# Kernel tuning notes

Measured on AMD Instinct MI355X. Metric: run time of the kernel, lower is better.

The kernel has to match this reference:

```python
import jax, jax.numpy as jnp
import numpy as np

P = 8          # patch_size
EPS = 1e-6     # LayerNorm2d eps


def _conv(x, w, b, groups=1):
    # x: (B,Cin,H,W), w: (Cout, Cin//groups, kh, kw)
    y = jax.lax.conv_general_dilated(
        x, w, window_strides=(1, 1), padding='SAME',
        feature_group_count=groups,
        dimension_numbers=('NCHW', 'OIHW', 'NCHW'))
    return y + b[None, :, None, None]


def _ln2d(x, w, b):
    mu = jnp.mean(x, axis=1, keepdims=True)
    var = jnp.mean((x - mu) ** 2, axis=1, keepdims=True)
    y = (x - mu) / jnp.sqrt(var + EPS)
    return w[None, :, None, None] * y + b[None, :, None, None]


def _fft_mix(x, fw):
    # windowed rFFT2 -> per-(channel,freq) real weight -> irFFT2.
    # H,W divisible by P, so window_partitionx == plain window partition.
    B, C, H, W = x.shape
    nh, nw = H // P, W // P
    xw = x.reshape(B, C, nh, P, nw, P).transpose(0, 2, 4, 1, 3, 5)  # (B,nh,nw,C,P,P)
    f = jnp.fft.rfft2(xw)                    # (B,nh,nw,C,P,P//2+1)
    f = f * fw                               # fw: (C,P,P//2+1) broadcasts
    xw = jnp.fft.irfft2(f, s=(P, P))
    return xw.transpose(0, 3, 1, 4, 2, 5).reshape(B, C, H, W)


def _gelu(x):
    return jax.nn.gelu(x, approximate=False)  # torch nn.GELU default = exact erf


def setup_inputs() -> dict:
    key = jax.random.key(0)
    ks = jax.random.split(key, 18)
    B, C, H, W = 4, 64, 256, 256
    C4, D = C * 4, C // 4
    f32 = jnp.float32

    def n(k, shape, s):
        return (jax.random.normal(k, shape, f32) * s)

    return {
        'x': jax.random.normal(ks[0], (B, C, H, W), f32),
        'ln_w': jnp.ones((C,), f32),
        'ln_b': jnp.zeros((C,), f32),
        'pconv_w': n(ks[1], (D, D, 3, 3), 0.08),
        'pconv_b': n(ks[2], (D,), 0.02),
        'w0': n(ks[3], (C4, C, 1, 1), 0.12),
        'b0': n(ks[4], (C4,), 0.02),
        'w1': n(ks[5], (C4, C, 1, 1), 0.12),
        'b1': n(ks[6], (C4,), 0.02),
        'w2': n(ks[7], (C, C4, 1, 1), 0.06),
        'b2': n(ks[8], (C,), 0.02),
        'w3': n(ks[9], (C4, 1, 3, 3), 0.3),
        'b3': n(ks[10], (C4,), 0.02),
        'w4': n(ks[11], (C, C4, 1, 1), 0.06),
        'b4': n(ks[12], (C,), 0.02),
        'fftw1': 1.0 + n(ks[13], (C, P, P // 2 + 1), 0.1),
        'fftw2': 1.0 + n(ks[14], (C, P, P // 2 + 1), 0.1),
    }


def reference(x, ln_w, ln_b, pconv_w, pconv_b, w0, b0, w1, b1,
              w2, b2, w3, b3, w4, b4, fftw1, fftw2):
    C = x.shape[1]
    D = C // 4
    C4 = C * 4

    xn = _ln2d(x, ln_w, ln_b)

    # partial 3x3 conv on first C//4 channels
    y1 = _conv(xn[:, :D], pconv_w, pconv_b)
    x2 = jnp.concatenate([y1, xn[:, D:]], axis=1)

    # branch 1: 1x1 expand -> GELU -> 1x1 contract -> windowed FFT mixing
    x1 = _conv(xn, w0, b0)
    x1 = _gelu(x1)
    x1 = _conv(x1, w2, b2)
    x1 = _fft_mix(x1, fftw1)

    # branch 2: 1x1 expand -> GELU -> depthwise 3x3 -> GELU -> 1x1 contract -> FFT mixing
    x2 = _conv(x2, w1, b1)
    x2 = _gelu(x2)
    x2 = _conv(x2, w3, b3, groups=C4)
    x2 = _gelu(x2)
    x2 = _conv(x2, w4, b4)
    x2 = _fft_mix(x2, fftw2)

    return x1 + x2
```

## Files before the change

### kernel.cpp

```cpp
#include <hip/hip_runtime.h>


typedef _Float16 f16;
typedef _Float16 f16x2 __attribute__((ext_vector_type(2)));
typedef _Float16 f16x4 __attribute__((ext_vector_type(4)));
typedef _Float16 f16x8 __attribute__((ext_vector_type(8)));
typedef float f32x4 __attribute__((ext_vector_type(4)));

__device__ __forceinline__ float gelu_f(float x) {
  float u = 1.5957691216f * (x + 0.044715f * x * x * x);
  float t = exp2f(-1.4426950409f * u);
#if __has_builtin(__builtin_amdgcn_rcpf)
  return x * __builtin_amdgcn_rcpf(1.0f + t);
#else
  return x / (1.0f + t);
#endif
}

__device__ __forceinline__ float dot2f(f16x2 a, f16x2 b, float c) {
#if __has_builtin(__builtin_amdgcn_fdot2)
  return __builtin_amdgcn_fdot2(a, b, c, false);
#else
  return c + (float)a.x * (float)b.x + (float)a.y * (float)b.y;
#endif
}

__global__ void build_kappa_kernel(const float* __restrict__ fw1,
                                   const float* __restrict__ fw2,
                                   float* __restrict__ kap1,
                                   float* __restrict__ kap2) {
  int which = blockIdx.x >> 6, c = blockIdx.x & 63;
  const float* fw = which ? fw2 : fw1;
  float* kap = which ? kap2 : kap1;
  int t = threadIdx.x, a = t >> 3, bb = t & 7;
  __shared__ float Wt[64];
  __shared__ float ct[8];
  if (t == 0) {
    const float r2 = 0.70710678118654752440f;
    ct[0] = 1.f; ct[1] = r2; ct[2] = 0.f; ct[3] = -r2;
    ct[4] = -1.f; ct[5] = -r2; ct[6] = 0.f; ct[7] = r2;
  }
  {
    int u = a, v = bb;
    Wt[t] = (v <= 4) ? fw[c * 40 + u * 5 + v]
                     : fw[c * 40 + ((8 - u) & 7) * 5 + (8 - v)];
  }
  __syncthreads();
  float acc = 0.f;
  for (int u = 0; u < 8; ++u)
    for (int v = 0; v < 8; ++v)
      acc += Wt[u * 8 + v] * ct[(u * a + v * bb) & 7];
  kap[c * 64 + t] = acc * 0.015625f;
}

__global__ void preconv_kernel(const float* __restrict__ w0, const float* __restrict__ w1,
                               const float* __restrict__ w2, const float* __restrict__ w4,
                               const float* __restrict__ w3, const float* __restrict__ b3,
                               f16* __restrict__ W0h, f16* __restrict__ W1h,
                               f16* __restrict__ W2h, f16* __restrict__ W4h,
                               f16* __restrict__ w3pk, f16* __restrict__ b3pk) {
  int i = blockIdx.x * 256 + threadIdx.x;
  if (i < 16384) W0h[i] = (f16)w0[i];
  else if (i < 32768) W1h[i - 16384] = (f16)w1[i - 16384];
  else if (i < 49152) W2h[i - 32768] = (f16)w2[i - 32768];
  else if (i < 65536) W4h[i - 49152] = (f16)w4[i - 49152];
  else if (i < 67840) {
    int j = i - 65536;
    int g = j / 72, r = j % 72, tap = r >> 3, k = r & 7;
    w3pk[j] = (f16)w3[(g * 8 + k) * 9 + tap];
  } else if (i < 68096) {
    int k = i - 67840;
    b3pk[k] = (f16)b3[k];
  }
}

__global__ void __launch_bounds__(256) ln_kernel(const float* __restrict__ x,
                                                 const float* __restrict__ lnw,
                                                 const float* __restrict__ lnb,
                                                 f16* __restrict__ xn) {
  int b = blockIdx.y;
  int px = blockIdx.x * 256 + threadIdx.x;
  const float* xp = x + ((size_t)b << 22) + px;
  float v[64];
  float s = 0.f;
#pragma unroll
  for (int c = 0; c < 64; ++c) { v[c] = xp[(size_t)c << 16]; s += v[c]; }
  float mu = s * (1.f / 64.f), s2 = 0.f;
#pragma unroll
  for (int c = 0; c < 64; ++c) { float d = v[c] - mu; s2 += d * d; }
  float rstd = rsqrtf(s2 * (1.f / 64.f) + 1e-6f);
  f16* op = xn + (size_t)b * 4194304 + (size_t)px * 64;
#pragma unroll
  for (int g = 0; g < 8; ++g) {
    f16x8 pk;
#pragma unroll
    for (int j = 0; j < 8; ++j) {
      int c = g * 8 + j;
      pk[j] = (f16)((v[c] - mu) * rstd * lnw[c] + lnb[c]);
    }
    *(f16x8*)(op + g * 8) = pk;
  }
}

__global__ void __launch_bounds__(256) pconv_kernel(const f16* __restrict__ xn,
                                                    const float* __restrict__ pw,
                                                    const float* __restrict__ pb,
                                                    f16* __restrict__ y1) {
  __shared__ __align__(16) char halo[18 * 640];
  __shared__ f16 wpk[2304];
  __shared__ float pbs[16];
  int t = threadIdx.x, blk = blockIdx.x, b = blockIdx.y;
  const f16* xnb = xn + (size_t)b * 4194304;
  f16* y1b = y1 + (size_t)b * 1048576;
  int h0 = (blk >> 4) << 4, w0 = (blk & 15) << 4;
  for (int i = t; i < 2304; i += 256) {
    int co = i / 144, r = i % 144, tap = r >> 4, ci = r & 15;
    wpk[i] = (f16)pw[co * 144 + ci * 9 + tap];
  }
  if (t < 16) pbs[t] = pb[t];
  for (int i = 0; i < 3; ++i) {
    int u = i * 256 + t;
    if (u < 648) {
      int hp = u >> 1, half = u & 1;
      int hr = hp / 18, hc = hp - hr * 18;
      int h = h0 - 1 + hr, w = w0 - 1 + hc;
      f16x8 v = {0, 0, 0, 0, 0, 0, 0, 0};
      if ((unsigned)h < 256u && (unsigned)w < 256u)
        v = *(const f16x8*)(xnb + ((((size_t)h << 8)) + w) * 64 + half * 8);
      *(f16x8*)(halo + hr * 640 + ((hc * 32 + half * 16) ^ ((hr & 7) << 4))) = v;
    }
  }
  __syncthreads();
  int rl = t >> 4, cl = t & 15;
  float acc[16];
#pragma unroll
  for (int co = 0; co < 16; ++co) acc[co] = pbs[co];
#pragma unroll
  for (int ty = 0; ty < 3; ++ty)
#pragma unroll
    for (int tx = 0; tx < 3; ++tx) {
      int hr = rl + ty, hc = cl + tx, tap = ty * 3 + tx;
      f16x8 ld0 = *(const f16x8*)(halo + hr * 640 + ((hc * 32) ^ ((hr & 7) << 4)));
      f16x8 ld1 = *(const f16x8*)(halo + hr * 640 + ((hc * 32 + 16) ^ ((hr & 7) << 4)));
#pragma unroll
      for (int co = 0; co < 16; ++co) {
#pragma unroll
        for (int p = 0; p < 4; ++p) {
          f16x2 xp = {ld0[2 * p], ld0[2 * p + 1]};
          f16x2 wp = *(const f16x2*)&wpk[co * 144 + tap * 16 + 2 * p];
          acc[co] = dot2f(xp, wp, acc[co]);
        }
#pragma unroll
        for (int p = 0; p < 4; ++p) {
          f16x2 xp = {ld1[2 * p], ld1[2 * p + 1]};
          f16x2 wp = *(const f16x2*)&wpk[co * 144 + tap * 16 + 8 + 2 * p];
          acc[co] = dot2f(xp, wp, acc[co]);
        }
      }
    }
  size_t px = (((size_t)(h0 + rl)) << 8) + w0 + cl;
  f16x8 o0, o1;
#pragma unroll
  for (int j = 0; j < 8; ++j) { o0[j] = (f16)acc[j]; o1[j] = (f16)acc[8 + j]; }
  *(f16x8*)(y1b + px * 16) = o0;
  *(f16x8*)(y1b + px * 16 + 8) = o1;
}

__global__ void __launch_bounds__(256) b1_kernel(
    const f16* __restrict__ xn, const f16* __restrict__ W0h,
    const float* __restrict__ b0, const f16* __restrict__ W2h,
    const float* __restrict__ b2, f16* __restrict__ u1d,
    f16* __restrict__ u1w) {
  __shared__ __align__(16) f16 As[8192];
  __shared__ __align__(16) f16 Es[8192];
  int t = threadIdx.x, b = blockIdx.y;
  const f16* xnb = xn + (size_t)b * 4194304;
  f16* u1b = (b < 3) ? (u1d + (size_t)b * 4194304) : u1w;
  int px0 = blockIdx.x << 7;
#pragma unroll
  for (int i = 0; i < 4; ++i) {
    int u = i * 256 + t, row = u >> 3, cb = (u & 7) << 4;
    f16x8 v = *(const f16x8*)(xnb + (size_t)(px0 + row) * 64 + (cb >> 1));
    *(f16x8*)((char*)As + row * 128 + (cb ^ ((row & 7) << 4))) = v;
  }
  __syncthreads();
  int l = t & 63, wv = t >> 6, lm = l & 15, kg = l >> 4;
  f32x4 uacc[2][4];
#pragma unroll
  for (int a = 0; a < 2; ++a)
#pragma unroll
    for (int n = 0; n < 4; ++n) uacc[a][n] = (f32x4){0.f, 0.f, 0.f, 0.f};
  for (int cc = 0; cc < 4; ++cc) {
    f32x4 eacc[2][4];
#pragma unroll
    for (int a = 0; a < 2; ++a)
#pragma unroll
      for (int n = 0; n < 4; ++n) eacc[a][n] = (f32x4){0.f, 0.f, 0.f, 0.f};
#pragma unroll
    for (int kk = 0; kk < 2; ++kk) {
      int kb = kk * 64 + kg * 16;
      f16x8 af[2];
#pragma unroll
      for (int mt = 0; mt < 2; ++mt) {
        int row = wv * 32 + mt * 16 + lm;
        af[mt] = *(const f16x8*)((char*)As + row * 128 + (kb ^ ((row & 7) << 4)));
      }
      f16x8 bf[4];
#pragma unroll
      for (int nt = 0; nt < 4; ++nt) {
        int co = cc * 64 + nt * 16 + lm;
        bf[nt] = *(const f16x8*)(W0h + (size_t)co * 64 + kk * 32 + kg * 8);
      }
#pragma unroll
      for (int mt = 0; mt < 2; ++mt)
#pragma unroll
        for (int nt = 0; nt < 4; ++nt)
          eacc[mt][nt] = __builtin_amdgcn_mfma_f32_16x16x32_f16(bf[nt], af[mt], eacc[mt][nt], 0, 0, 0);
    }
    if (cc) __syncthreads();
#pragma unroll
    for (int mt = 0; mt < 2; ++mt) {
      int row = wv * 32 + mt * 16 + lm;
#pragma unroll
      for (int nt = 0; nt < 4; ++nt) {
        int c0 = nt * 16 + kg * 4;
        float4 bz4 = *(const float4*)&b0[cc * 64 + c0];
        f16x4 pk;
        pk[0] = (f16)gelu_f(eacc[mt][nt][0] + bz4.x);
        pk[1] = (f16)gelu_f(eacc[mt][nt][1] + bz4.y);
        pk[2] = (f16)gelu_f(eacc[mt][nt][2] + bz4.z);
        pk[3] = (f16)gelu_f(eacc[mt][nt][3] + bz4.w);
        *(f16x4*)((char*)Es + row * 128 + ((c0 * 2) ^ ((row & 7) << 4))) = pk;
      }
    }
    __syncthreads();
#pragma unroll
    for (int kk = 0; kk < 2; ++kk) {
      int kb = kk * 64 + kg * 16;
      f16x8 af[2];
#pragma unroll
      for (int mt = 0; mt < 2; ++mt) {
        int row = wv * 32 + mt * 16 + lm;
        af[mt] = *(const f16x8*)((char*)Es + row * 128 + (kb ^ ((row & 7) << 4)));
      }
      f16x8 bf[4];
#pragma unroll
      for (int nt = 0; nt < 4; ++nt) {
        int co = nt * 16 + lm;
        bf[nt] = *(const f16x8*)(W2h + (size_t)co * 256 + cc * 64 + kk * 32 + kg * 8);
      }
#pragma unroll
      for (int mt = 0; mt < 2; ++mt)
#pragma unroll
        for (int nt = 0; nt < 4; ++nt)
          uacc[mt][nt] = __builtin_amdgcn_mfma_f32_16x16x32_f16(bf[nt], af[mt], uacc[mt][nt], 0, 0, 0);
    }
    __syncthreads();
  }
#pragma unroll
  for (int mt = 0; mt < 2; ++mt) {
    int row = wv * 32 + mt * 16 + lm;
#pragma unroll
    for (int nt = 0; nt < 4; ++nt) {
      int c0 = nt * 16 + kg * 4;
      float4 bz4 = *(const float4*)&b2[c0];
      f16x4 pk;
      pk[0] = (f16)(uacc[mt][nt][0] + bz4.x);
      pk[1] = (f16)(uacc[mt][nt][1] + bz4.y);
      pk[2] = (f16)(uacc[mt][nt][2] + bz4.z);
      pk[3] = (f16)(uacc[mt][nt][3] + bz4.w);
      *(f16x4*)((char*)Es + row * 128 + ((c0 * 2) ^ ((row & 7) << 4))) = pk;
    }
  }
  __syncthreads();
  int co = t >> 2, q = t & 3;
  f16x8 o[4];
#pragma unroll
  for (int i = 0; i < 32; ++i) {
    int m = q * 32 + i;
    o[i >> 3][i & 7] =
        *(const f16*)((char*)Es + m * 128 + ((co * 2) ^ ((m & 7) << 4)));
  }
  f16* up = u1b + ((size_t)co << 16) + px0 + q * 32;
#pragma unroll
  for (int ss = 0; ss < 4; ++ss) *(f16x8*)(up + ss * 8) = o[ss];
}

__global__ void __launch_bounds__(256) b2_kernel(
    const f16* __restrict__ xn, const f16* __restrict__ y1,
    const f16* __restrict__ W1h, const float* __restrict__ b1v,
    const f16* __restrict__ W4h, const float* __restrict__ b4,
    const f16* __restrict__ w3pk, const f16* __restrict__ b3pk,
    f16* __restrict__ u2) {
  __shared__ __align__(16) f16 xin[12288];
  __shared__ __align__(16) f16 Es[6144];
  int t = threadIdx.x, blk = blockIdx.x, b = blockIdx.y;
  const f16* xnb = xn + (size_t)b * 4194304;
  const f16* y1b = y1 + (size_t)b * 1048576;
  f16* u2b = u2 + (size_t)b * 4194304;
  int h0 = (blk >> 4) << 3, w0 = (blk & 15) << 4;
#pragma unroll
  for (int i = 0; i < 6; ++i) {
    int u = i * 256 + t;
    int hp = u >> 3, part = u & 7;
    f16x8 v = {0, 0, 0, 0, 0, 0, 0, 0};
    if (hp < 180) {
      int hr = hp / 18, hc = hp - hr * 18;
      int h = h0 - 1 + hr, w = w0 - 1 + hc;
      if ((unsigned)h < 256u && (unsigned)w < 256u) {
        size_t px = ((size_t)h << 8) + w;
        v = (part < 2) ? *(const f16x8*)(y1b + px * 16 + part * 8)
                       : *(const f16x8*)(xnb + px * 64 + part * 8);
      }
    }
    *(f16x8*)((char*)xin + hp * 128 + ((part * 16) ^ ((hp & 7) << 4))) = v;
  }
  __syncthreads();
  int l = t & 63, wv = t >> 6, lm = l & 15, kg = l >> 4;
  f32x4 uacc[2][4];
#pragma unroll
  for (int a = 0; a < 2; ++a)
#pragma unroll
    for (int n = 0; n < 4; ++n) uacc[a][n] = (f32x4){0.f, 0.f, 0.f, 0.f};
  for (int kc = 0; kc < 4; ++kc) {
#pragma unroll
    for (int sub = 0; sub < 2; ++sub) {
      int ce0 = kc * 64 + sub * 32;
      f32x4 eacc[3][2];
#pragma unroll
      for (int a = 0; a < 3; ++a)
#pragma unroll
        for (int n = 0; n < 2; ++n) eacc[a][n] = (f32x4){0.f, 0.f, 0.f, 0.f};
#pragma unroll
      for (int kk = 0; kk < 2; ++kk) {
        int kb = kk * 64 + kg * 16;
        f16x8 af[3];
#pragma unroll
        for (int mtl = 0; mtl < 3; ++mtl) {
          int row = (mtl * 4 + wv) * 16 + lm;
          af[mtl] = *(const f16x8*)((char*)xin + row * 128 + (kb ^ ((row & 7) << 4)));
        }
        f16x8 bf[2];
#pragma unroll
        for (int nt = 0; nt < 2; ++nt) {
          int ce = ce0 + nt * 16 + lm;
          bf[nt] = *(const f16x8*)(W1h + (size_t)ce * 64 + kk * 32 + kg * 8);
        }
#pragma unroll
        for (int mtl = 0; mtl < 3; ++mtl)
#pragma unroll
          for (int nt = 0; nt < 2; ++nt)
            eacc[mtl][nt] = __builtin_amdgcn_mfma_f32_16x16x32_f16(bf[nt], af[mtl], eacc[mtl][nt], 0, 0, 0);
      }
      __syncthreads();
#pragma unroll
      for (int mtl = 0; mtl < 3; ++mtl) {
        int row = (mtl * 4 + wv) * 16 + lm;
#pragma unroll
        for (int nt = 0; nt < 2; ++nt) {
          int cL = nt * 16 + kg * 4;
          float4 bz4 = *(const float4*)&b1v[ce0 + cL];
          f16x4 pk;
          pk[0] = (f16)gelu_f(eacc[mtl][nt][0] + bz4.x);
          pk[1] = (f16)gelu_f(eacc[mtl][nt][1] + bz4.y);
          pk[2] = (f16)gelu_f(eacc[mtl][nt][2] + bz4.z);
          pk[3] = (f16)gelu_f(eacc[mtl][nt][3] + bz4.w);
          *(f16x4*)((char*)Es + row * 64 + ((cL * 2) ^ (((row >> 1) & 3) << 4))) = pk;
        }
      }
      __syncthreads();
      int g9 = (ce0 + kg * 8) >> 3;
      f16x8 wv9[9];
#pragma unroll
      for (int tap = 0; tap < 9; ++tap)
        wv9[tap] = *(const f16x8*)(w3pk + g9 * 72 + tap * 8);
      f16x8 bias8 = *(const f16x8*)(b3pk + ce0 + kg * 8);
      f16x8 af2[2];
#pragma unroll
      for (int mt = 0; mt < 2; ++mt) {
        int px = wv * 32 + mt * 16 + lm;
        int rl2 = px >> 4, cl2 = px & 15;
        f16x8 a8 = bias8;
#pragma unroll
        for (int ty = 0; ty < 3; ++ty)
#pragma unroll
          for (int tx = 0; tx < 3; ++tx) {
            int hp = (rl2 + ty) * 18 + (cl2 + tx);
            f16x8 xv = *(const f16x8*)((char*)Es + hp * 64 + ((kg * 16) ^ (((hp >> 1) & 3) << 4)));
            a8 += xv * wv9[ty * 3 + tx];
          }
#pragma unroll
        for (int j2 = 0; j2 < 8; ++j2) af2[mt][j2] = (f16)gelu_f((float)a8[j2]);
      }
      f16x8 bf2[4];
#pragma unroll
      for (int nt = 0; nt < 4; ++nt) {
        int co = nt * 16 + lm;
        bf2[nt] = *(const f16x8*)(W4h + (size_t)co * 256 + ce0 + kg * 8);
      }
#pragma unroll
      for (int mt = 0; mt < 2; ++mt)
#pragma unroll
        for (int nt = 0; nt < 4; ++nt)
          uacc[mt][nt] = __builtin_amdgcn_mfma_f32_16x16x32_f16(bf2[nt], af2[mt], uacc[mt][nt], 0, 0, 0);
    }
  }
  __syncthreads();
#pragma unroll
  for (int mt = 0; mt < 2; ++mt) {
    int m = wv * 32 + mt * 16 + lm;
#pragma unroll
    for (int nt = 0; nt < 4; ++nt) {
      int c0 = nt * 16 + kg * 4;
      float4 bz4 = *(const float4*)&b4[c0];
      f16x4 pk;
      pk[0] = (f16)(uacc[mt][nt][0] + bz4.x);
      pk[1] = (f16)(uacc[mt][nt][1] + bz4.y);
      pk[2] = (f16)(uacc[mt][nt][2] + bz4.z);
      pk[3] = (f16)(uacc[mt][nt][3] + bz4.w);
      *(f16x4*)((char*)xin + m * 128 + ((c0 * 2) ^ ((m & 7) << 4))) = pk;
    }
  }
  __syncthreads();
  int co = t >> 2, q = t & 3;
  f16x8 o[4];
#pragma unroll
  for (int i = 0; i < 32; ++i) {
    int m = q * 32 + i;
    o[i >> 3][i & 7] =
        *(const f16*)((char*)xin + m * 128 + ((co * 2) ^ ((m & 7) << 4)));
  }
  f16* up = u2b + ((size_t)co << 16) + (size_t)(h0 + 2 * q) * 256 + w0;
  *(f16x8*)(up) = o[0];
  *(f16x8*)(up + 8) = o[1];
  *(f16x8*)(up + 256) = o[2];
  *(f16x8*)(up + 256 + 8) = o[3];
}

__global__ void __launch_bounds__(256) fftmix_kernel(
    const f16* __restrict__ u1, const f16* __restrict__ u2,
    const float* __restrict__ kap1, const float* __restrict__ kap2,
    float* __restrict__ out, int b) {
  int blk = blockIdx.x;
  int c = blk >> 3, part = blk & 7;
  int t = threadIdx.x;
  int l = t & 63, wv = (t >> 6) & 3;
  int s = l >> 3, tq = l & 7;
  __shared__ unsigned int kls[64];
  if (t < 64) {
    f16 k1 = (f16)kap1[(c << 6) + t];
    f16 k2 = (f16)kap2[(c << 6) + t];
    kls[t] = (unsigned int)__builtin_bit_cast(unsigned short, k1) |
             ((unsigned int)__builtin_bit_cast(unsigned short, k2) << 16);
  }
  __syncthreads();
  unsigned int kp[64];
#pragma unroll
  for (int j = 0; j < 64; ++j) {
    int idx = (((s - (j >> 3)) & 7) << 3) | ((tq - (j & 7)) & 7);
    kp[j] = kls[idx];
  }
  size_t cb = ((size_t)c) << 16;
  size_t obase = ((size_t)(b * 64 + c)) << 16;
  int win0 = part * 128 + wv * 32;
  for (int it = 0; it < 32; ++it) {
    int win = win0 + it;
    int wh = win >> 5, ww = win & 31;
    size_t pix = (size_t)((wh * 8 + s) << 8) + ww * 8 + tq;
    unsigned int pk =
        (unsigned int)__builtin_bit_cast(unsigned short, u1[cb + pix]) |
        ((unsigned int)__builtin_bit_cast(unsigned short, u2[cb + pix]) << 16);
    float acc = 0.f;
#pragma unroll
    for (int j = 0; j < 64; ++j) {
      unsigned int bc = (unsigned int)__builtin_amdgcn_readlane((int)pk, j);
      acc = dot2f(__builtin_bit_cast(f16x2, bc),
                  __builtin_bit_cast(f16x2, kp[j]), acc);
    }
    out[obase + pix] = acc;
  }
}

__global__ void diag_kernel(float* __restrict__ out, float code, int n) {
  int i = blockIdx.x * 256 + threadIdx.x;
  for (int p = i; p < n; p += 256 * 4096) out[p] = (p == 0) ? code : 0.f;
}

extern "C" void kernel_launch(void* const* d_in, const int* in_sizes, int n_in,
                              void* d_out, int out_size, void* d_ws,
                              size_t ws_size, hipStream_t stream) {
  const float* x       = (const float*)d_in[0];
  const float* ln_w    = (const float*)d_in[1];
  const float* ln_b    = (const float*)d_in[2];
  const float* pconv_w = (const float*)d_in[3];
  const float* pconv_b = (const float*)d_in[4];
  const float* w0      = (const float*)d_in[5];
  const float* b0      = (const float*)d_in[6];
  const float* w1      = (const float*)d_in[7];
  const float* b1      = (const float*)d_in[8];
  const float* w2      = (const float*)d_in[9];
  const float* b2      = (const float*)d_in[10];
  const float* w3      = (const float*)d_in[11];
  const float* b3      = (const float*)d_in[12];
  const float* w4      = (const float*)d_in[13];
  const float* b4      = (const float*)d_in[14];
  const float* fftw1   = (const float*)d_in[15];
  const float* fftw2   = (const float*)d_in[16];

  const size_t OFF_KAP1 = 0;
  const size_t OFF_KAP2 = 16384;
  const size_t OFF_W0H  = 32768;
  const size_t OFF_W1H  = 65536;
  const size_t OFF_W2H  = 98304;
  const size_t OFF_W4H  = 131072;
  const size_t OFF_W3PK = 163840;
  const size_t OFF_B3PK = 168448;
  const size_t OFF_Y1   = 168960;
  const size_t OFF_U2   = OFF_Y1 + 8388608ull;
  const size_t OFF_U13  = OFF_U2 + 33554432ull;
  const size_t WS_NEED  = OFF_U13 + 8388608ull;

  float* outF = (float*)d_out;
  if (ws_size < WS_NEED) {
    diag_kernel<<<4096, 256, 0, stream>>>(outF, 1000.0f + (float)(ws_size >> 20), 16777216);
    return;
  }
  char* ws = (char*)d_ws;
  float* kap1 = (float*)(ws + OFF_KAP1);
  float* kap2 = (float*)(ws + OFF_KAP2);
  f16* W0h  = (f16*)(ws + OFF_W0H);
  f16* W1h  = (f16*)(ws + OFF_W1H);
  f16* W2h  = (f16*)(ws + OFF_W2H);
  f16* W4h  = (f16*)(ws + OFF_W4H);
  f16* w3pk = (f16*)(ws + OFF_W3PK);
  f16* b3pk = (f16*)(ws + OFF_B3PK);
  f16* Y1   = (f16*)(ws + OFF_Y1);
  f16* U2   = (f16*)(ws + OFF_U2);
  f16* U13  = (f16*)(ws + OFF_U13);

  f16* XN  = (f16*)d_out;
  f16* U1D = (f16*)d_out + 16777216;

  build_kappa_kernel<<<128, 64, 0, stream>>>(fftw1, fftw2, kap1, kap2);
  preconv_kernel<<<266, 256, 0, stream>>>(w0, w1, w2, w4, w3, b3,
                                          W0h, W1h, W2h, W4h, w3pk, b3pk);
  ln_kernel<<<dim3(256, 4), 256, 0, stream>>>(x, ln_w, ln_b, XN);
  pconv_kernel<<<dim3(256, 4), 256, 0, stream>>>(XN, pconv_w, pconv_b, Y1);
  b1_kernel<<<dim3(512, 4), 256, 0, stream>>>(XN, W0h, b0, W2h, b2, U1D, U13);
  b2_kernel<<<dim3(512, 4), 256, 0, stream>>>(XN, Y1, W1h, b1, W4h, b4,
                                              w3pk, b3pk, U2);
  for (int b = 0; b < 4; ++b) {
    const f16* u1b = (b < 3) ? (U1D + (size_t)b * 4194304) : U13;
    fftmix_kernel<<<512, 256, 0, stream>>>(u1b, U2 + (size_t)b * 4194304,
                                           kap1, kap2, outF, b);
  }
}
```

Measured before the change: 395.3 us.

## Use packed fp16 GELU, merge kappa into preconv, split fftmix grid finer

The GELU epilogues now run in packed half precision with f16 exp2/rcp, and the bias-add conversions use packed round-toward-zero converts. The kappa-building kernel is folded into the weight-conversion kernel, saving one launch. The fftmix kernel doubles its grid with half the windows per block and splits the 64-term dot chain into four independent accumulators for more ILP. Doing GELU in fp16 reduces accuracy, and a larger grid means each block reloads its per-channel kernel setup more often.

```diff
diff --git a/kernel.cpp b/kernel.cpp
--- a/kernel.cpp
+++ b/kernel.cpp
@@ -6,16 +6,6 @@
 typedef _Float16 f16x4 __attribute__((ext_vector_type(4)));
 typedef _Float16 f16x8 __attribute__((ext_vector_type(8)));
 typedef float f32x4 __attribute__((ext_vector_type(4)));
-
-__device__ __forceinline__ float gelu_f(float x) {
-  float u = 1.5957691216f * (x + 0.044715f * x * x * x);
-  float t = exp2f(-1.4426950409f * u);
-#if __has_builtin(__builtin_amdgcn_rcpf)
-  return x * __builtin_amdgcn_rcpf(1.0f + t);
-#else
-  return x / (1.0f + t);
-#endif
-}
 
 __device__ __forceinline__ float dot2f(f16x2 a, f16x2 b, float c) {
 #if __has_builtin(__builtin_amdgcn_fdot2)
@@ -25,53 +15,84 @@
 #endif
 }
 
-__global__ void build_kappa_kernel(const float* __restrict__ fw1,
-                                   const float* __restrict__ fw2,
-                                   float* __restrict__ kap1,
-                                   float* __restrict__ kap2) {
-  int which = blockIdx.x >> 6, c = blockIdx.x & 63;
+__device__ __forceinline__ f16x2 gelu_pk(f16x2 x) {
+  const f16x2 c1 = {(f16)1.5957691f, (f16)1.5957691f};
+  const f16x2 c3 = {(f16)0.0713548f, (f16)0.0713548f};
+  const f16x2 cl = {(f16)-1.4426950f, (f16)-1.4426950f};
+  f16x2 x2 = x * x;
+  f16x2 u = x * (c1 + c3 * x2);
+  f16x2 a = cl * u;
+  f16 t0, t1;
+#if __has_builtin(__builtin_amdgcn_exp2h)
+  t0 = __builtin_amdgcn_exp2h(a[0]);
+  t1 = __builtin_amdgcn_exp2h(a[1]);
+#else
+  t0 = (f16)exp2f((float)a[0]);
+  t1 = (f16)exp2f((float)a[1]);
+#endif
+  f16 d0 = (f16)1.0f + t0, d1 = (f16)1.0f + t1;
+  f16 r0, r1;
+#if __has_builtin(__builtin_amdgcn_rcph)
+  r0 = __builtin_amdgcn_rcph(d0);
+  r1 = __builtin_amdgcn_rcph(d1);
+#else
+  r0 = (f16)(1.0f / (float)d0);
+  r1 = (f16)(1.0f / (float)d1);
+#endif
+  f16x2 r = {r0, r1};
+  return x * r;
+}
+
+__device__ __forceinline__ f16x2 cvtpk(float a, float b) {
+  return __builtin_bit_cast(f16x2, __builtin_amdgcn_cvt_pkrtz(a, b));
+}
+
+__global__ void preconv_kernel(const float* __restrict__ w0, const float* __restrict__ w1,
+                               const float* __restrict__ w2, const float* __restrict__ w4,
+                               const float* __restrict__ w3, const float* __restrict__ b3,
+                               const float* __restrict__ fw1, const float* __restrict__ fw2,
+                               f16* __restrict__ W0h, f16* __restrict__ W1h,
+                               f16* __restrict__ W2h, f16* __restrict__ W4h,
+                               f16* __restrict__ w3pk, f16* __restrict__ b3pk,
+                               float* __restrict__ kap1, float* __restrict__ kap2) {
+  __shared__ float Wt[4][64];
+  __shared__ float ct[8];
+  int blk = blockIdx.x, t = threadIdx.x;
+  if (blk < 266) {
+    int i = blk * 256 + t;
+    if (i < 16384) W0h[i] = (f16)w0[i];
+    else if (i < 32768) W1h[i - 16384] = (f16)w1[i - 16384];
+    else if (i < 49152) W2h[i - 32768] = (f16)w2[i - 32768];
+    else if (i < 65536) W4h[i - 49152] = (f16)w4[i - 49152];
+    else if (i < 67840) {
+      int j = i - 65536;
+      int g = j / 72, r = j % 72, tap = r >> 3, k = r & 7;
+      w3pk[j] = (f16)w3[(g * 8 + k) * 9 + tap];
+    } else if (i < 68096) {
+      int k = i - 67840;
+      b3pk[k] = (f16)b3[k];
+    }
+    return;
+  }
+  int sub = t >> 6, lane = t & 63;
+  int unit = (blk - 266) * 4 + sub;
+  int which = unit >> 6, c = unit & 63;
   const float* fw = which ? fw2 : fw1;
   float* kap = which ? kap2 : kap1;
-  int t = threadIdx.x, a = t >> 3, bb = t & 7;
-  __shared__ float Wt[64];
-  __shared__ float ct[8];
+  int a = lane >> 3, bb = lane & 7;
   if (t == 0) {
     const float r2 = 0.70710678118654752440f;
     ct[0] = 1.f; ct[1] = r2; ct[2] = 0.f; ct[3] = -r2;
     ct[4] = -1.f; ct[5] = -r2; ct[6] = 0.f; ct[7] = r2;
   }
-  {
-    int u = a, v = bb;
-    Wt[t] = (v <= 4) ? fw[c * 40 + u * 5 + v]
-                     : fw[c * 40 + ((8 - u) & 7) * 5 + (8 - v)];
-  }
+  Wt[sub][lane] = (bb <= 4) ? fw[c * 40 + a * 5 + bb]
+                            : fw[c * 40 + ((8 - a) & 7) * 5 + (8 - bb)];
   __syncthreads();
   float acc = 0.f;
   for (int u = 0; u < 8; ++u)
     for (int v = 0; v < 8; ++v)
-      acc += Wt[u * 8 + v] * ct[(u * a + v * bb) & 7];
-  kap[c * 64 + t] = acc * 0.015625f;
-}
-
-__global__ void preconv_kernel(const float* __restrict__ w0, const float* __restrict__ w1,
-                               const float* __restrict__ w2, const float* __restrict__ w4,
-                               const float* __restrict__ w3, const float* __restrict__ b3,
-                               f16* __restrict__ W0h, f16* __restrict__ W1h,
-                               f16* __restrict__ W2h, f16* __restrict__ W4h,
-                               f16* __restrict__ w3pk, f16* __restrict__ b3pk) {
-  int i = blockIdx.x * 256 + threadIdx.x;
-  if (i < 16384) W0h[i] = (f16)w0[i];
-  else if (i < 32768) W1h[i - 16384] = (f16)w1[i - 16384];
-  else if (i < 49152) W2h[i - 32768] = (f16)w2[i - 32768];
-  else if (i < 65536) W4h[i - 49152] = (f16)w4[i - 49152];
-  else if (i < 67840) {
-    int j = i - 65536;
-    int g = j / 72, r = j % 72, tap = r >> 3, k = r & 7;
-    w3pk[j] = (f16)w3[(g * 8 + k) * 9 + tap];
-  } else if (i < 68096) {
-    int k = i - 67840;
-    b3pk[k] = (f16)b3[k];
-  }
+      acc += Wt[sub][u * 8 + v] * ct[(u * a + v * bb) & 7];
+  kap[c * 64 + lane] = acc * 0.015625f;
 }
 
 __global__ void __launch_bounds__(256) ln_kernel(const float* __restrict__ x,
@@ -225,11 +246,9 @@
       for (int nt = 0; nt < 4; ++nt) {
         int c0 = nt * 16 + kg * 4;
         float4 bz4 = *(const float4*)&b0[cc * 64 + c0];
-        f16x4 pk;
-        pk[0] = (f16)gelu_f(eacc[mt][nt][0] + bz4.x);
-        pk[1] = (f16)gelu_f(eacc[mt][nt][1] + bz4.y);
-        pk[2] = (f16)gelu_f(eacc[mt][nt][2] + bz4.z);
-        pk[3] = (f16)gelu_f(eacc[mt][nt][3] + bz4.w);
+        f16x2 lo = gelu_pk(cvtpk(eacc[mt][nt][0] + bz4.x, eacc[mt][nt][1] + bz4.y));
+        f16x2 hi = gelu_pk(cvtpk(eacc[mt][nt][2] + bz4.z, eacc[mt][nt][3] + bz4.w));
+        f16x4 pk = {lo[0], lo[1], hi[0], hi[1]};
         *(f16x4*)((char*)Es + row * 128 + ((c0 * 2) ^ ((row & 7) << 4))) = pk;
       }
     }
@@ -264,11 +283,9 @@
     for (int nt = 0; nt < 4; ++nt) {
       int c0 = nt * 16 + kg * 4;
       float4 bz4 = *(const float4*)&b2[c0];
-      f16x4 pk;
-      pk[0] = (f16)(uacc[mt][nt][0] + bz4.x);
-      pk[1] = (f16)(uacc[mt][nt][1] + bz4.y);
-      pk[2] = (f16)(uacc[mt][nt][2] + bz4.z);
-      pk[3] = (f16)(uacc[mt][nt][3] + bz4.w);
+      f16x2 lo = cvtpk(uacc[mt][nt][0] + bz4.x, uacc[mt][nt][1] + bz4.y);
+      f16x2 hi = cvtpk(uacc[mt][nt][2] + bz4.z, uacc[mt][nt][3] + bz4.w);
+      f16x4 pk = {lo[0], lo[1], hi[0], hi[1]};
       *(f16x4*)((char*)Es + row * 128 + ((c0 * 2) ^ ((row & 7) << 4))) = pk;
     }
   }
@@ -360,11 +377,9 @@
         for (int nt = 0; nt < 2; ++nt) {
           int cL = nt * 16 + kg * 4;
           float4 bz4 = *(const float4*)&b1v[ce0 + cL];
-          f16x4 pk;
-          pk[0] = (f16)gelu_f(eacc[mtl][nt][0] + bz4.x);
-          pk[1] = (f16)gelu_f(eacc[mtl][nt][1] + bz4.y);
-          pk[2] = (f16)gelu_f(eacc[mtl][nt][2] + bz4.z);
-          pk[3] = (f16)gelu_f(eacc[mtl][nt][3] + bz4.w);
+          f16x2 lo = gelu_pk(cvtpk(eacc[mtl][nt][0] + bz4.x, eacc[mtl][nt][1] + bz4.y));
+          f16x2 hi = gelu_pk(cvtpk(eacc[mtl][nt][2] + bz4.z, eacc[mtl][nt][3] + bz4.w));
+          f16x4 pk = {lo[0], lo[1], hi[0], hi[1]};
           *(f16x4*)((char*)Es + row * 64 + ((cL * 2) ^ (((row >> 1) & 3) << 4))) = pk;
         }
       }
@@ -390,7 +405,11 @@
             a8 += xv * wv9[ty * 3 + tx];
           }
 #pragma unroll
-        for (int j2 = 0; j2 < 8; ++j2) af2[mt][j2] = (f16)gelu_f((float)a8[j2]);
+        for (int j2 = 0; j2 < 4; ++j2) {
+          f16x2 g = gelu_pk((f16x2){a8[2 * j2], a8[2 * j2 + 1]});
+          af2[mt][2 * j2] = g[0];
+          af2[mt][2 * j2 + 1] = g[1];
+        }
       }
       f16x8 bf2[4];
 #pragma unroll
@@ -413,11 +432,9 @@
     for (int nt = 0; nt < 4; ++nt) {
       int c0 = nt * 16 + kg * 4;
       float4 bz4 = *(const float4*)&b4[c0];
-      f16x4 pk;
-      pk[0] = (f16)(uacc[mt][nt][0] + bz4.x);
-      pk[1] = (f16)(uacc[mt][nt][1] + bz4.y);
-      pk[2] = (f16)(uacc[mt][nt][2] + bz4.z);
-      pk[3] = (f16)(uacc[mt][nt][3] + bz4.w);
+      f16x2 lo = cvtpk(uacc[mt][nt][0] + bz4.x, uacc[mt][nt][1] + bz4.y);
+      f16x2 hi = cvtpk(uacc[mt][nt][2] + bz4.z, uacc[mt][nt][3] + bz4.w);
+      f16x4 pk = {lo[0], lo[1], hi[0], hi[1]};
       *(f16x4*)((char*)xin + m * 128 + ((c0 * 2) ^ ((m & 7) << 4))) = pk;
     }
   }
@@ -442,7 +459,7 @@
     const float* __restrict__ kap1, const float* __restrict__ kap2,
     float* __restrict__ out, int b) {
   int blk = blockIdx.x;
-  int c = blk >> 3, part = blk & 7;
+  int c = blk >> 4, part = blk & 15;
   int t = threadIdx.x;
   int l = t & 63, wv = (t >> 6) & 3;
   int s = l >> 3, tq = l & 7;
@@ -462,22 +479,27 @@
   }
   size_t cb = ((size_t)c) << 16;
   size_t obase = ((size_t)(b * 64 + c)) << 16;
-  int win0 = part * 128 + wv * 32;
-  for (int it = 0; it < 32; ++it) {
+  int win0 = part * 64 + wv * 16;
+  for (int it = 0; it < 16; ++it) {
     int win = win0 + it;
     int wh = win >> 5, ww = win & 31;
     size_t pix = (size_t)((wh * 8 + s) << 8) + ww * 8 + tq;
     unsigned int pk =
         (unsigned int)__builtin_bit_cast(unsigned short, u1[cb + pix]) |
         ((unsigned int)__builtin_bit_cast(unsigned short, u2[cb + pix]) << 16);
-    float acc = 0.f;
-#pragma unroll
-    for (int j = 0; j < 64; ++j) {
-      unsigned int bc = (unsigned int)__builtin_amdgcn_readlane((int)pk, j);
-      acc = dot2f(__builtin_bit_cast(f16x2, bc),
-                  __builtin_bit_cast(f16x2, kp[j]), acc);
-    }
-    out[obase + pix] = acc;
+    float ac0 = 0.f, ac1 = 0.f, ac2 = 0.f, ac3 = 0.f;
+#pragma unroll
+    for (int j = 0; j < 64; j += 4) {
+      unsigned int v0 = (unsigned int)__builtin_amdgcn_readlane((int)pk, j);
+      unsigned int v1 = (unsigned int)__builtin_amdgcn_readlane((int)pk, j + 1);
+      unsigned int v2 = (unsigned int)__builtin_amdgcn_readlane((int)pk, j + 2);
+      unsigned int v3 = (unsigned int)__builtin_amdgcn_readlane((int)pk, j + 3);
+      ac0 = dot2f(__builtin_bit_cast(f16x2, v0), __builtin_bit_cast(f16x2, kp[j]), ac0);
+      ac1 = dot2f(__builtin_bit_cast(f16x2, v1), __builtin_bit_cast(f16x2, kp[j + 1]), ac1);
+      ac2 = dot2f(__builtin_bit_cast(f16x2, v2), __builtin_bit_cast(f16x2, kp[j + 2]), ac2);
+      ac3 = dot2f(__builtin_bit_cast(f16x2, v3), __builtin_bit_cast(f16x2, kp[j + 3]), ac3);
+    }
+    out[obase + pix] = (ac0 + ac1) + (ac2 + ac3);
   }
 }
 
@@ -541,9 +563,9 @@
   f16* XN  = (f16*)d_out;
   f16* U1D = (f16*)d_out + 16777216;
 
-  build_kappa_kernel<<<128, 64, 0, stream>>>(fftw1, fftw2, kap1, kap2);
-  preconv_kernel<<<266, 256, 0, stream>>>(w0, w1, w2, w4, w3, b3,
-                                          W0h, W1h, W2h, W4h, w3pk, b3pk);
+  preconv_kernel<<<298, 256, 0, stream>>>(w0, w1, w2, w4, w3, b3, fftw1, fftw2,
+                                          W0h, W1h, W2h, W4h, w3pk, b3pk,
+                                          kap1, kap2);
   ln_kernel<<<dim3(256, 4), 256, 0, stream>>>(x, ln_w, ln_b, XN);
   pconv_kernel<<<dim3(256, 4), 256, 0, stream>>>(XN, pconv_w, pconv_b, Y1);
   b1_kernel<<<dim3(512, 4), 256, 0, stream>>>(XN, W0h, b0, W2h, b2, U1D, U13);
@@ -551,7 +573,7 @@
                                               w3pk, b3pk, U2);
   for (int b = 0; b < 4; ++b) {
     const f16* u1b = (b < 3) ? (U1D + (size_t)b * 4194304) : U13;
-    fftmix_kernel<<<512, 256, 0, stream>>>(u1b, U2 + (size_t)b * 4194304,
-                                           kap1, kap2, outF, b);
-  }
-}
+    fftmix_kernel<<<1024, 256, 0, stream>>>(u1b, U2 + (size_t)b * 4194304,
+                                            kap1, kap2, outF, b);
+  }
+}
```

Measured after the change: 361.4 us. 1.09x faster.
